# Kernel tuning notes

Hardware: AMD Instinct MI355X
Metric: run time of the kernel (lower is better)

The kernel has to match this reference:

```python
import jax, jax.numpy as jnp
import numpy as np

B, T, C = 4, 2048, 1024
H = 16
D = C // H  # head_dim = 64

def setup_inputs() -> dict:
    key = jax.random.key(0)
    k1, k2, k3 = jax.random.split(key, 3)
    x = jax.random.normal(k1, (B, T, C), dtype=jnp.float32)
    Wqkv = jax.random.normal(k2, (C, 3 * C), dtype=jnp.float32) * (C ** -0.5)
    Wproj = jax.random.normal(k3, (C, C), dtype=jnp.float32) * (C ** -0.5)
    return {"x": x, "Wqkv": Wqkv, "Wproj": Wproj}

def reference(x, Wqkv, Wproj):
    b, t, c = x.shape
    qkv = (x @ Wqkv).reshape(b, t, 3, H, D)
    qkv = jnp.transpose(qkv, (2, 0, 3, 1, 4))  # [3, B, H, T, D]
    q, k, v = qkv[0], qkv[1], qkv[2]
    att = jnp.einsum('bhqd,bhkd->bhqk', q, k) * (D ** -0.5)
    causal = jnp.tril(jnp.ones((t, t), dtype=bool))  # True where allowed
    att = jnp.where(causal, att, -jnp.inf)
    att = jax.nn.softmax(att, axis=-1)
    out = jnp.einsum('bhqk,bhkd->bhqd', att, v)  # [B, H, T, D]
    out = jnp.transpose(out, (0, 2, 1, 3)).reshape(b, t, c)
    return out @ Wproj
```

## Files before the change

kernel.cpp:

```cpp
#include <hip/hip_runtime.h>
#include <stdint.h>

typedef unsigned short u16;
typedef __bf16 bf16x8 __attribute__((ext_vector_type(8)));
typedef float f32x4 __attribute__((ext_vector_type(4)));

#define DEVI static __device__ __forceinline__

DEVI u16 f2bf(float f) {
  union { float f; unsigned u; } v; v.f = f;
  unsigned r = v.u + 0x7FFF + ((v.u >> 16) & 1);
  return (u16)(r >> 16);
}

DEVI unsigned pkbf(float a, float b) {
  union { float f; unsigned u; } x, y; x.f = a; y.f = b;
  return __builtin_amdgcn_perm(y.u + 0x8000u, x.u + 0x8000u, 0x07060302u);
}

DEVI void gl2lds16(const u16* g, u16* l) {
  __builtin_amdgcn_global_load_lds(
      (const __attribute__((address_space(1))) unsigned int*)(uintptr_t)g,
      (__attribute__((address_space(3))) unsigned int*)(uintptr_t)l,
      16, 0, 0);
}

__global__ __launch_bounds__(256)
void convert_f32_bf16(const float* __restrict__ in, u16* __restrict__ out) {
  const int i = blockIdx.x * 256 + threadIdx.x;
  const float4 v = ((const float4*)in)[i];
  ushort4 o;
  o.x = f2bf(v.x); o.y = f2bf(v.y); o.z = f2bf(v.z); o.w = f2bf(v.w);
  ((ushort4*)out)[i] = o;
}

__global__ __launch_bounds__(256)
void transpose_bf16(const float* __restrict__ in, u16* __restrict__ out,
                    int R, int Cn) {
  __shared__ float tile[64][65];
  const int n0 = blockIdx.x * 64;
  const int r0 = blockIdx.y * 64;
#pragma unroll
  for (int i = 0; i < 16; ++i) {
    const int e = threadIdx.x + i * 256;
    const int r = e >> 6, c = e & 63;
    tile[r][c] = in[(size_t)(r0 + r) * Cn + n0 + c];
  }
  __syncthreads();
#pragma unroll
  for (int i = 0; i < 16; ++i) {
    const int e = threadIdx.x + i * 256;
    const int r = e >> 6, c = e & 63;
    out[(size_t)(n0 + r) * R + r0 + c] = f2bf(tile[c][r]);
  }
}

template <int MODE>
__global__ __launch_bounds__(256)
void gemm128(const u16* __restrict__ A, const u16* __restrict__ Bt,
             int M, int N, int K, float* __restrict__ Cout,
             u16* __restrict__ Qg, u16* __restrict__ Kg, u16* __restrict__ Vtg) {
  __shared__ alignas(16) u16 As[128 * 32];
  __shared__ alignas(16) u16 Bs[128 * 32];
  const int tid = threadIdx.x;
  const int wave = tid >> 6, lane = tid & 63;
  const int quad = lane >> 4, l15 = lane & 15;
  const int m0 = blockIdx.y * 128;
  const int n0 = blockIdx.x * 128;
  const int wm = (wave >> 1) * 64;
  const int wn = (wave & 1) * 64;

  f32x4 acc[4][4] = {};

  const int q1 = wave * 64 + lane;
  const int q2 = q1 + 256;
  const int r1 = q1 >> 2, c1 = q1 & 3;
  const int r2 = q2 >> 2, c2 = q2 & 3;

  for (int k0 = 0; k0 < K; k0 += 32) {
    __syncthreads();
    gl2lds16(A + (size_t)(m0 + r1) * K + k0 + c1 * 8, As + wave * 512);
    gl2lds16(A + (size_t)(m0 + r2) * K + k0 + c2 * 8, As + 2048 + wave * 512);
    gl2lds16(Bt + (size_t)(n0 + r1) * K + k0 + c1 * 8, Bs + wave * 512);
    gl2lds16(Bt + (size_t)(n0 + r2) * K + k0 + c2 * 8, Bs + 2048 + wave * 512);
    __syncthreads();
    bf16x8 av[4], bv[4];
#pragma unroll
    for (int i = 0; i < 4; ++i)
      av[i] = *(const bf16x8*)(As + (wm + i * 16 + l15) * 32 + quad * 8);
#pragma unroll
    for (int j = 0; j < 4; ++j)
      bv[j] = *(const bf16x8*)(Bs + (wn + j * 16 + l15) * 32 + quad * 8);
#pragma unroll
    for (int i = 0; i < 4; ++i)
#pragma unroll
      for (int j = 0; j < 4; ++j)
        acc[i][j] = __builtin_amdgcn_mfma_f32_16x16x32_bf16(av[i], bv[j], acc[i][j], 0, 0, 0);
  }

  if constexpr (MODE == 0) {
#pragma unroll
    for (int i = 0; i < 4; ++i) {
#pragma unroll
      for (int j = 0; j < 4; ++j) {
        const int mb = m0 + wm + i * 16 + quad * 4;
        const int n = n0 + wn + j * 16 + l15;
#pragma unroll
        for (int r = 0; r < 4; ++r)
          Cout[(size_t)(mb + r) * N + n] = acc[i][j][r];
      }
    }
  } else {
    const int s0b = n0 >> 10;
    const int b = m0 >> 11;
    const int h = ((n0 + wn) >> 6) & 15;
    const int bh = b * 16 + h;
    const int tbase = (m0 & 2047) + wm;
    if (s0b == 2) {
      __syncthreads();
      u16* sl = (wave < 2 ? As : Bs) + (wave & 1) * 2048;
#pragma unroll
      for (int jp = 0; jp < 2; ++jp) {
#pragma unroll
        for (int j2 = 0; j2 < 2; ++j2) {
          const int j = jp * 2 + j2;
          const int dl = j2 * 16 + l15;
          const int sw8 = dl & 7;
#pragma unroll
          for (int i = 0; i < 4; ++i) {
            const int tq = i * 2 + (quad >> 1);
            ushort4 pk;
            pk.x = f2bf(acc[i][j][0]); pk.y = f2bf(acc[i][j][1]);
            pk.z = f2bf(acc[i][j][2]); pk.w = f2bf(acc[i][j][3]);
            *(ushort4*)(sl + dl * 64 + ((tq ^ sw8) << 3) + (quad & 1) * 4) = pk;
          }
        }
#pragma unroll
        for (int p = 0; p < 4; ++p) {
          const int dl = p * 8 + (lane >> 3);
          const int tc = lane & 7;
          const int tcu = tc ^ (dl & 7);
          const uint4 v = *(const uint4*)(sl + dl * 64 + tc * 8);
          *(uint4*)(Vtg + ((size_t)(bh * 64 + jp * 32 + dl)) * 2048 + tbase + tcu * 8) = v;
        }
      }
    } else {
      u16* dst = s0b ? Kg : Qg;
      const float scale = s0b ? 1.0f : 0.18033688f;
#pragma unroll
      for (int i = 0; i < 4; ++i) {
        const int t0 = tbase + i * 16 + quad * 4;
#pragma unroll
        for (int j = 0; j < 4; ++j) {
          const int d = j * 16 + l15;
#pragma unroll
          for (int r = 0; r < 4; ++r)
            dst[((size_t)bh * 2048 + t0 + r) * 64 + d] = f2bf(acc[i][j][r] * scale);
        }
      }
    }
  }
}

__global__ __launch_bounds__(256)
void attn_fwd(const u16* __restrict__ Qg, const u16* __restrict__ Kg,
              const u16* __restrict__ Vtg, u16* __restrict__ Og) {
  __shared__ alignas(16) u16 Ks[64 * 64];
  __shared__ alignas(16) u16 Vts[64 * 64];
  __shared__ alignas(16) u16 Ps[4][16 * 64];

  const int tid = threadIdx.x;
  const int wave = tid >> 6, lane = tid & 63;
  const int quad = lane >> 4, l15 = lane & 15;
  const int bh = blockIdx.x & 63;
  const int qt = 15 - (blockIdx.x >> 6);
  const int b = bh >> 4, h = bh & 15;
  const int sw = l15 & 7;

  const int rs0 = wave * 16 + (lane >> 3);
  const int rs1 = rs0 + 8;
  const int cs = (lane & 7) ^ (rs0 & 7);
  const size_t kgb0 = (size_t)(bh * 2048 + rs0) * 64 + cs * 8;
  const size_t kgb1 = (size_t)(bh * 2048 + rs1) * 64 + cs * 8;
  const size_t vgb0 = (size_t)(bh * 64 + rs0) * 2048 + cs * 8;
  const size_t vgb1 = (size_t)(bh * 64 + rs1) * 2048 + cs * 8;
  const int ldsw0 = wave * 1024;
  const int ldsw1 = wave * 1024 + 512;

  const int qb0 = qt * 128 + wave * 32;

  bf16x8 bq[2][2];
#pragma unroll
  for (int qs = 0; qs < 2; ++qs)
#pragma unroll
    for (int hv = 0; hv < 2; ++hv)
      bq[qs][hv] = *(const bf16x8*)(Qg + ((size_t)bh * 2048 + qb0 + qs * 16 + l15) * 64 + hv * 32 + quad * 8);

  f32x4 oacc[2][4] = {};
  float li[2] = {0.f, 0.f};

  const int jlast = qt * 128 + 64;
  for (int j0 = 0; j0 <= jlast; j0 += 64) {
    __syncthreads();
    gl2lds16(Kg + kgb0 + (size_t)j0 * 64, Ks + ldsw0);
    gl2lds16(Kg + kgb1 + (size_t)j0 * 64, Ks + ldsw1);
    gl2lds16(Vtg + vgb0 + j0, Vts + ldsw0);
    gl2lds16(Vtg + vgb1 + j0, Vts + ldsw1);
    __syncthreads();
    if (j0 > qb0 + 31) continue;

    bf16x8 aK[4][2];
#pragma unroll
    for (int ks = 0; ks < 4; ++ks)
#pragma unroll
      for (int hv = 0; hv < 2; ++hv)
        aK[ks][hv] = *(const bf16x8*)(Ks + (ks * 16 + l15) * 64 + ((hv * 4 + quad) ^ sw) * 8);
    bf16x8 bV[4][2];
#pragma unroll
    for (int ds = 0; ds < 4; ++ds)
#pragma unroll
      for (int kc = 0; kc < 2; ++kc)
        bV[ds][kc] = *(const bf16x8*)(Vts + (ds * 16 + l15) * 64 + ((kc * 4 + quad) ^ sw) * 8);

#pragma unroll
    for (int qs = 0; qs < 2; ++qs) {
      const int qb = qb0 + qs * 16;
      if (j0 > qb + 15) continue;
      u16* Pw = Ps[wave];
      const bool needmask = (j0 + 63 > qb);
#pragma unroll
      for (int ks = 0; ks < 4; ++ks) {
        f32x4 s = {};
        s = __builtin_amdgcn_mfma_f32_16x16x32_bf16(aK[ks][0], bq[qs][0], s, 0, 0, 0);
        s = __builtin_amdgcn_mfma_f32_16x16x32_bf16(aK[ks][1], bq[qs][1], s, 0, 0, 0);
        if (needmask) {
          const int kbase = j0 + ks * 16 + quad * 4;
          const int qrow = qb + l15;
#pragma unroll
          for (int r = 0; r < 4; ++r)
            if (kbase + r > qrow) s[r] = -1e30f;
        }
        float p0 = __builtin_amdgcn_exp2f(s[0]);
        float p1 = __builtin_amdgcn_exp2f(s[1]);
        float p2 = __builtin_amdgcn_exp2f(s[2]);
        float p3 = __builtin_amdgcn_exp2f(s[3]);
        li[qs] += (p0 + p1) + (p2 + p3);
        uint2 pk;
        pk.x = pkbf(p0, p1);
        pk.y = pkbf(p2, p3);
        *(uint2*)(Pw + l15 * 64 + (((ks * 2 + (quad >> 1)) ^ sw) * 8) + (quad & 1) * 4) = pk;
      }
      bf16x8 aP0 = *(const bf16x8*)(Pw + l15 * 64 + ((0 * 4 + quad) ^ sw) * 8);
      bf16x8 aP1 = *(const bf16x8*)(Pw + l15 * 64 + ((1 * 4 + quad) ^ sw) * 8);
#pragma unroll
      for (int ds = 0; ds < 4; ++ds) {
        oacc[qs][ds] = __builtin_amdgcn_mfma_f32_16x16x32_bf16(aP0, bV[ds][0], oacc[qs][ds], 0, 0, 0);
        oacc[qs][ds] = __builtin_amdgcn_mfma_f32_16x16x32_bf16(aP1, bV[ds][1], oacc[qs][ds], 0, 0, 0);
      }
    }
  }

#pragma unroll
  for (int qs = 0; qs < 2; ++qs) {
    float l = li[qs];
    l += __shfl_xor(l, 16);
    l += __shfl_xor(l, 32);
    const int qb = qb0 + qs * 16;
#pragma unroll
    for (int r = 0; r < 4; ++r) {
      const float lrow = __shfl(l, quad * 4 + r);
      const float inv = 1.0f / lrow;
      u16* orow = Og + ((size_t)b * 2048 + qb + quad * 4 + r) * 1024 + h * 64;
#pragma unroll
      for (int ds = 0; ds < 4; ++ds)
        orow[ds * 16 + l15] = f2bf(oacc[qs][ds][r] * inv);
    }
  }
}

extern "C" void kernel_launch(void* const* d_in, const int* in_sizes, int n_in,
                              void* d_out, int out_size, void* d_ws, size_t ws_size,
                              hipStream_t stream) {
  const float* x = (const float*)d_in[0];
  const float* Wqkv = (const float*)d_in[1];
  const float* Wproj = (const float*)d_in[2];
  float* out = (float*)d_out;

  char* ws = (char*)d_ws;
  u16* xb     = (u16*)(ws);
  u16* wqkvT  = (u16*)(ws + 16777216);
  u16* wprojT = (u16*)(ws + 23068672);
  u16* Qg     = (u16*)(ws + 25165824);
  u16* Kg     = (u16*)(ws + 41943040);
  u16* Vtg    = (u16*)(ws + 58720256);
  u16* Og     = (u16*)(ws + 75497472);

  convert_f32_bf16<<<8192, 256, 0, stream>>>(x, xb);
  transpose_bf16<<<dim3(48, 16), 256, 0, stream>>>(Wqkv, wqkvT, 1024, 3072);
  transpose_bf16<<<dim3(16, 16), 256, 0, stream>>>(Wproj, wprojT, 1024, 1024);
  gemm128<1><<<dim3(24, 64), 256, 0, stream>>>(xb, wqkvT, 8192, 3072, 1024,
                                               nullptr, Qg, Kg, Vtg);
  attn_fwd<<<1024, 256, 0, stream>>>(Qg, Kg, Vtg, Og);
  gemm128<0><<<dim3(8, 64), 256, 0, stream>>>(Og, wprojT, 8192, 1024, 1024,
                                              out, nullptr, nullptr, nullptr);
}
```

Baseline: 257.8 us.

## Merge prep kernels into one launch and add LDS wait fences

The x conversion and the two weight transposes now run in a single kernel that dispatches on block index, replacing three launches with one. Explicit s_waitcnt lgkmcnt(0) fences are also placed around the per-wave LDS scratch write/read sequences in the V-transpose epilogue and in the attention P staging. The fences are meant to guarantee ordering between the intra-wave LDS writes and the following reads, which may have been a correctness hazard. They add stalls on LDS latency in exchange.

After: 257.7 us. No clear change (-0.1%).

```diff
diff --git a/kernel.cpp b/kernel.cpp
--- a/kernel.cpp
+++ b/kernel.cpp
@@ -17,6 +17,8 @@
   union { float f; unsigned u; } x, y; x.f = a; y.f = b;
   return __builtin_amdgcn_perm(y.u + 0x8000u, x.u + 0x8000u, 0x07060302u);
 }
+
+DEVI void lds_fence() { asm volatile("s_waitcnt lgkmcnt(0)" ::: "memory"); }
 
 DEVI void gl2lds16(const u16* g, u16* l) {
   __builtin_amdgcn_global_load_lds(
@@ -26,20 +28,29 @@
 }
 
 __global__ __launch_bounds__(256)
-void convert_f32_bf16(const float* __restrict__ in, u16* __restrict__ out) {
-  const int i = blockIdx.x * 256 + threadIdx.x;
-  const float4 v = ((const float4*)in)[i];
-  ushort4 o;
-  o.x = f2bf(v.x); o.y = f2bf(v.y); o.z = f2bf(v.z); o.w = f2bf(v.w);
-  ((ushort4*)out)[i] = o;
-}
-
-__global__ __launch_bounds__(256)
-void transpose_bf16(const float* __restrict__ in, u16* __restrict__ out,
-                    int R, int Cn) {
+void prep(const float* __restrict__ x, u16* __restrict__ xb,
+          const float* __restrict__ Wqkv, u16* __restrict__ wqkvT,
+          const float* __restrict__ Wproj, u16* __restrict__ wprojT) {
   __shared__ float tile[64][65];
-  const int n0 = blockIdx.x * 64;
-  const int r0 = blockIdx.y * 64;
+  const int blk = blockIdx.x;
+  if (blk < 8192) {
+    const int i = blk * 256 + threadIdx.x;
+    const float4 v = ((const float4*)x)[i];
+    ushort4 o;
+    o.x = f2bf(v.x); o.y = f2bf(v.y); o.z = f2bf(v.z); o.w = f2bf(v.w);
+    ((ushort4*)xb)[i] = o;
+    return;
+  }
+  const float* in; u16* out; int Cn, n0, r0;
+  if (blk < 8960) {
+    const int p = blk - 8192;
+    in = Wqkv; out = wqkvT; Cn = 3072;
+    n0 = (p % 48) * 64; r0 = (p / 48) * 64;
+  } else {
+    const int p = blk - 8960;
+    in = Wproj; out = wprojT; Cn = 1024;
+    n0 = (p % 16) * 64; r0 = (p / 16) * 64;
+  }
 #pragma unroll
   for (int i = 0; i < 16; ++i) {
     const int e = threadIdx.x + i * 256;
@@ -51,7 +62,7 @@
   for (int i = 0; i < 16; ++i) {
     const int e = threadIdx.x + i * 256;
     const int r = e >> 6, c = e & 63;
-    out[(size_t)(n0 + r) * R + r0 + c] = f2bf(tile[c][r]);
+    out[(size_t)(n0 + r) * 1024 + r0 + c] = f2bf(tile[c][r]);
   }
 }
 
@@ -135,6 +146,7 @@
             *(ushort4*)(sl + dl * 64 + ((tq ^ sw8) << 3) + (quad & 1) * 4) = pk;
           }
         }
+        lds_fence();
 #pragma unroll
         for (int p = 0; p < 4; ++p) {
           const int dl = p * 8 + (lane >> 3);
@@ -143,6 +155,7 @@
           const uint4 v = *(const uint4*)(sl + dl * 64 + tc * 8);
           *(uint4*)(Vtg + ((size_t)(bh * 64 + jp * 32 + dl)) * 2048 + tbase + tcu * 8) = v;
         }
+        lds_fence();
       }
     } else {
       u16* dst = s0b ? Kg : Qg;
@@ -250,6 +263,7 @@
         pk.y = pkbf(p2, p3);
         *(uint2*)(Pw + l15 * 64 + (((ks * 2 + (quad >> 1)) ^ sw) * 8) + (quad & 1) * 4) = pk;
       }
+      lds_fence();
       bf16x8 aP0 = *(const bf16x8*)(Pw + l15 * 64 + ((0 * 4 + quad) ^ sw) * 8);
       bf16x8 aP1 = *(const bf16x8*)(Pw + l15 * 64 + ((1 * 4 + quad) ^ sw) * 8);
 #pragma unroll
@@ -257,6 +271,7 @@
         oacc[qs][ds] = __builtin_amdgcn_mfma_f32_16x16x32_bf16(aP0, bV[ds][0], oacc[qs][ds], 0, 0, 0);
         oacc[qs][ds] = __builtin_amdgcn_mfma_f32_16x16x32_bf16(aP1, bV[ds][1], oacc[qs][ds], 0, 0, 0);
       }
+      lds_fence();
     }
   }
 
@@ -295,9 +310,7 @@
   u16* Vtg    = (u16*)(ws + 58720256);
   u16* Og     = (u16*)(ws + 75497472);
 
-  convert_f32_bf16<<<8192, 256, 0, stream>>>(x, xb);
-  transpose_bf16<<<dim3(48, 16), 256, 0, stream>>>(Wqkv, wqkvT, 1024, 3072);
-  transpose_bf16<<<dim3(16, 16), 256, 0, stream>>>(Wproj, wprojT, 1024, 1024);
+  prep<<<9216, 256, 0, stream>>>(x, xb, Wqkv, wqkvT, Wproj, wprojT);
   gemm128<1><<<dim3(24, 64), 256, 0, stream>>>(xb, wqkvT, 8192, 3072, 1024,
                                                nullptr, Qg, Kg, Vtg);
   attn_fwd<<<1024, 256, 0, stream>>>(Qg, Kg, Vtg, Og);
```
